# Optimization experiments

Measured on AMD Instinct MI355X. Metric: run time of the kernel, lower is better.

## Reference

```python
import jax, jax.numpy as jnp
import numpy as np

B, T, W_DIM = 32, 2048, 1024
G, D = 16, 64          # num_groups, input_dim (w = G*D)
MOM = 0.9
TH = 0.5
EPS = 1e-8
TOP_K = 2


def setup_inputs() -> dict:
    key = jax.random.key(0)
    k = jax.random.split(key, 4)
    x = jax.random.normal(k[0], (B, T, W_DIM), dtype=jnp.float32)
    ema = jnp.zeros((W_DIM, W_DIM), dtype=jnp.float32)
    W1 = jax.random.normal(k[1], (G, 16, D), dtype=jnp.float32) * 0.05
    b1 = jnp.zeros((G, 16), dtype=jnp.float32)
    W2 = jax.random.normal(k[2], (G, 1, 16), dtype=jnp.float32) * 0.05
    b2 = jnp.zeros((G, 1), dtype=jnp.float32)
    return {"x": x, "ema": ema, "W1": W1, "b1": b1, "W2": W2, "b2": b2}


def _corr_over_T(x):
    # x: (B, T, w) -> per-batch Pearson corr over the T axis: (B, w, w)
    Tn = x.shape[1]
    c = x - x.mean(axis=1, keepdims=True)
    cov = jnp.einsum('btw,btv->bwv', c, c) / (Tn - 1)
    std = jnp.sqrt(jnp.sum(c * c, axis=1) / (Tn - 1))  # (B, w)
    return jnp.clip(cov / (std[:, :, None] * std[:, None, :] + EPS), -1.0, 1.0)


def reference(x, ema, W1, b1, W2, b2):
    # --- burst-masked EMA update (torch.no_grad) ---
    corr_batch = jax.lax.stop_gradient(_corr_over_T(x))  # (B, w, w)

    def step(e, c):
        mask = jnp.abs(c) > TH
        return jnp.where(mask, MOM * e + (1.0 - MOM) * c, e), None

    ema_new, _ = jax.lax.scan(step, ema, corr_batch)

    # --- split into groups: (B, T, G, D) ---
    Bn, Tn, w = x.shape
    groups = x.reshape(Bn, Tn, G, D)

    # --- per-group correlation score: mean |off-diagonal| of within-group corr ---
    cg = groups - groups.mean(axis=1, keepdims=True)
    cov_g = jnp.einsum('btgd,btge->bgde', cg, cg) / (Tn - 1)        # (B, G, D, D)
    std_g = jnp.sqrt(jnp.sum(cg * cg, axis=1) / (Tn - 1))           # (B, G, D)
    corr_g = jnp.clip(cov_g / (std_g[..., :, None] * std_g[..., None, :] + EPS), -1.0, 1.0)
    absc = jnp.abs(corr_g)
    offdiag = (absc.sum(axis=(-2, -1)) - jnp.einsum('bgdd->bg', absc)) / (D * D - D)
    correlations = offdiag.mean(axis=0)                              # (G,)

    # --- select the 2 least-correlated groups (these get gradients) ---
    _, sel = jax.lax.top_k(-correlations, TOP_K)
    sel_mask = jnp.zeros((G,), dtype=bool).at[sel].set(True)

    # --- per-group expert MLP: D -> 16 -> 1, batched over groups ---
    h = jax.nn.relu(jnp.einsum('btgd,ghd->btgh', groups, W1) + b1)   # (B, T, G, 16)
    o = (jnp.einsum('btgh,goh->btgo', h, W2) + b2)[..., 0]           # (B, T, G)

    # non-selected groups run under no_grad -> stop_gradient on their outputs
    out = jnp.where(sel_mask[None, None, :], o, jax.lax.stop_gradient(o))
    return out, correlations, ema_new
```

## Files before the change

kernel.cpp:

```cpp
#include <hip/hip_runtime.h>
#include <hip/hip_bf16.h>
#include <stdint.h>

#define B_   32
#define T_   2048
#define W_   1024
#define G_   16
#define D_   64
#define LIST_CAP 65536

typedef __bf16 bf16_t;
typedef __bf16 bf16x8 __attribute__((ext_vector_type(8)));
typedef float  f32x4  __attribute__((ext_vector_type(4)));

#define WS_XT      0ull
#define WS_XT_SZ   (134217728ull)
#define WS_SUM     (WS_XT + WS_XT_SZ)
#define WS_SQ      (WS_SUM + 131072ull)
#define WS_MU      (WS_SQ  + 131072ull)
#define WS_SIG     (WS_MU  + 131072ull)
#define WS_ACCUM   (WS_SIG + 131072ull)
#define WS_LISTCNT (WS_ACCUM + 256ull)
#define WS_LIST    (WS_LISTCNT + 256ull)
#define WS_MASK    (WS_LIST + 1048576ull)
#define WS_DIAG    (WS_MASK + 4194304ull)

__global__ __launch_bounds__(256) void stats_transpose(
    const float* __restrict__ x, bf16_t* __restrict__ xT,
    float* __restrict__ sumb, float* __restrict__ sqb) {
  int b = blockIdx.z, t0 = blockIdx.x * 64, w0 = blockIdx.y * 64;
  __shared__ float tile[64][65];
  __shared__ float red[2][256];
  int tid = threadIdx.x;
  int c = tid & 63, r0 = tid >> 6;
  float ps = 0.f, pq = 0.f;
  const float* xp = x + ((size_t)b * T_ + t0) * W_ + w0 + c;
#pragma unroll
  for (int r = r0; r < 64; r += 4) {
    float v = xp[(size_t)r * W_];
    ps += v; pq += v * v;
    tile[c][r] = v;
  }
  red[0][tid] = ps; red[1][tid] = pq;
  __syncthreads();
  if (tid < 64) {
    float s = red[0][tid] + red[0][tid + 64] + red[0][tid + 128] + red[0][tid + 192];
    float q = red[1][tid] + red[1][tid + 64] + red[1][tid + 128] + red[1][tid + 192];
    atomicAdd(&sumb[b * W_ + w0 + tid], s);
    atomicAdd(&sqb[b * W_ + w0 + tid], q);
  }
  int tl = tid & 63, wl0 = tid >> 6;
  bf16_t* xtp = xT + ((size_t)b * W_ + w0) * T_ + t0 + tl;
#pragma unroll
  for (int wl = wl0; wl < 64; wl += 4)
    xtp[(size_t)wl * T_] = (bf16_t)tile[wl][tl];
}

__global__ void finalize_stats(const float* __restrict__ sumb,
                               const float* __restrict__ sqb,
                               float* __restrict__ mu, float* __restrict__ sig) {
  int idx = blockIdx.x * 256 + threadIdx.x;
  float s = sumb[idx], q = sqb[idx];
  float m = s * (1.0f / 2048.0f);
  float var = (q - s * m) * (1.0f / 2047.0f);
  if (var < 0.f) var = 0.f;
  mu[idx] = m;
  sig[idx] = sqrtf(var);
}

__global__ __launch_bounds__(256) void gram_kernel(
    const bf16_t* __restrict__ xT, const float* __restrict__ mu,
    const float* __restrict__ sig, unsigned int* __restrict__ mask,
    float* __restrict__ diagv, int* __restrict__ listcnt,
    int4* __restrict__ list, float* __restrict__ accum) {
  int b = blockIdx.y;
  int r = blockIdx.x, ti = 0;
  while (r >= 8 - ti) { r -= 8 - ti; ++ti; }
  int tj = ti + r;
  int i0 = ti * 128, j0 = tj * 128;

  const bf16_t* Ag = xT + ((size_t)b * W_ + i0) * T_;
  const bf16_t* Bg = xT + ((size_t)b * W_ + j0) * T_;

  __shared__ __attribute__((aligned(16))) bf16_t As[128 * 32];
  __shared__ __attribute__((aligned(16))) bf16_t Bs[128 * 32];

  int tid = threadIdx.x;
  int lane = tid & 63, wave = tid >> 6;
  int wm = wave >> 1, wn = wave & 1;

  f32x4 zero = {0.f, 0.f, 0.f, 0.f};
  f32x4 acc[4][4];
#pragma unroll
  for (int mi = 0; mi < 4; ++mi)
#pragma unroll
    for (int nj = 0; nj < 4; ++nj) acc[mi][nj] = zero;

  int aoff = (wm * 64 + (lane & 15)) * 32 + (lane >> 4) * 8;
  int boff = (wn * 64 + (lane & 15)) * 32 + (lane >> 4) * 8;

  for (int k0 = 0; k0 < T_; k0 += 32) {
    __syncthreads();
#pragma unroll
    for (int s = 0; s < 2; ++s) {
      int chunk = s * 256 + tid;
      int row = chunk >> 2, kc = (chunk & 3) * 8;
      __builtin_amdgcn_global_load_lds(
          (const __attribute__((address_space(1))) void*)(Ag + (size_t)row * T_ + k0 + kc),
          (__attribute__((address_space(3))) void*)(As + chunk * 8), 16, 0, 0);
      __builtin_amdgcn_global_load_lds(
          (const __attribute__((address_space(1))) void*)(Bg + (size_t)row * T_ + k0 + kc),
          (__attribute__((address_space(3))) void*)(Bs + chunk * 8), 16, 0, 0);
    }
    __syncthreads();

    bf16x8 af[4], bfr[4];
#pragma unroll
    for (int mi = 0; mi < 4; ++mi) af[mi]  = *(const bf16x8*)(As + aoff + mi * 512);
#pragma unroll
    for (int nj = 0; nj < 4; ++nj) bfr[nj] = *(const bf16x8*)(Bs + boff + nj * 512);
#pragma unroll
    for (int mi = 0; mi < 4; ++mi)
#pragma unroll
      for (int nj = 0; nj < 4; ++nj)
        acc[mi][nj] = __builtin_amdgcn_mfma_f32_16x16x32_bf16(af[mi], bfr[nj], acc[mi][nj], 0, 0, 0);
  }

  const float inv = 1.0f / 2047.0f;
  const float* mub = mu + b * W_;
  const float* sgb = sig + b * W_;
  bool diagquad = (ti == tj) && (wm == wn);
  float gsum = 0.f;

#pragma unroll
  for (int nj = 0; nj < 4; ++nj) {
    int j = j0 + wn * 64 + nj * 16 + (lane & 15);
    float muj = mub[j], sgj = sgb[j];
#pragma unroll
    for (int mi = 0; mi < 4; ++mi) {
#pragma unroll
      for (int rr = 0; rr < 4; ++rr) {
        int i = i0 + wm * 64 + mi * 16 + (lane >> 4) * 4 + rr;
        float cov = (acc[mi][nj][rr] - 2048.0f * mub[i] * muj) * inv;
        float corr = cov / (sgb[i] * sgj + 1e-8f);
        corr = fminf(1.0f, fmaxf(-1.0f, corr));
        if (diagquad && (i != j)) gsum += fabsf(corr);
        if (fabsf(corr) > 0.5f) {
          atomicOr(&mask[i * W_ + j], 1u << b);
          if (i == j) {
            diagv[b * W_ + i] = corr;
          } else {
            int p = atomicAdd(listcnt, 1);
            if (p < LIST_CAP) list[p] = make_int4(b, i, j, __float_as_int(corr));
          }
          if (ti != tj) {
            atomicOr(&mask[j * W_ + i], 1u << b);
            int p = atomicAdd(listcnt, 1);
            if (p < LIST_CAP) list[p] = make_int4(b, j, i, __float_as_int(corr));
          }
        }
      }
    }
  }
  if (diagquad) {
    for (int o = 32; o > 0; o >>= 1) gsum += __shfl_down(gsum, o);
    if (lane == 0) atomicAdd(&accum[ti * 2 + wm], gsum);
  }
}

__global__ void ema_kernel(const float* __restrict__ ema,
                           const unsigned int* __restrict__ mask,
                           const float* __restrict__ diagv,
                           const int* __restrict__ listcnt,
                           const int4* __restrict__ list,
                           float* __restrict__ emaout) {
  int idx = blockIdx.x * 256 + threadIdx.x;
  int i = idx >> 10, j = idx & 1023;
  float e = ema[idx];
  unsigned int m = mask[idx];
  if (m) {
    if (i == j) {
      for (int b = 0; b < 32; ++b)
        if ((m >> b) & 1u) e = 0.9f * e + 0.1f * diagv[b * W_ + i];
    } else {
      int cnt = *listcnt; if (cnt > LIST_CAP) cnt = LIST_CAP;
      for (int b = 0; b < 32; ++b) {
        if ((m >> b) & 1u) {
          for (int k = 0; k < cnt; ++k) {
            int4 t = list[k];
            if (t.x == b && t.y == i && t.z == j) {
              e = 0.9f * e + 0.1f * __int_as_float(t.w);
              break;
            }
          }
        }
      }
    }
  }
  emaout[idx] = e;
}

__global__ void corr_finalize(const float* __restrict__ accum, float* __restrict__ outc) {
  int g = threadIdx.x;
  if (g < 16) outc[g] = accum[g] * (1.0f / (32.0f * 4032.0f));
}

__global__ __launch_bounds__(256) void mlp_kernel(
    const float* __restrict__ x, const float* __restrict__ W1,
    const float* __restrict__ b1, const float* __restrict__ W2,
    const float* __restrict__ b2, float* __restrict__ out) {
  int b = blockIdx.y, t0 = blockIdx.x * 64, gs = blockIdx.z * 4;
  int tid = threadIdx.x;
  int gl = tid & 3, tl = tid >> 2;
  __shared__ float Wt[16 * 64 * 4];
  __shared__ float b1s[16 * 4], W2s[16 * 4], b2s[4];
  for (int l = tid; l < 4096; l += 256) {
    int g2 = l & 3, jd = l >> 2;
    Wt[l] = W1[(size_t)(gs + g2) * 1024 + jd];
  }
  if (tid < 64) {
    int g2 = tid & 3, j = tid >> 2;
    b1s[j * 4 + g2] = b1[(gs + g2) * 16 + j];
    W2s[j * 4 + g2] = W2[(gs + g2) * 16 + j];
  }
  if (tid < 4) b2s[tid] = b2[gs + tid];
  __syncthreads();

  int g = gs + gl, t = t0 + tl;
  const float4* xp = (const float4*)(x + ((size_t)b * T_ + t) * W_ + g * D_);
  float h[16];
#pragma unroll
  for (int j = 0; j < 16; ++j) h[j] = b1s[j * 4 + gl];
#pragma unroll
  for (int d4 = 0; d4 < 16; ++d4) {
    float4 xv = xp[d4];
#pragma unroll
    for (int j = 0; j < 16; ++j) {
      const float* wp = &Wt[(j * 64 + d4 * 4) * 4 + gl];
      h[j] += xv.x * wp[0] + xv.y * wp[4] + xv.z * wp[8] + xv.w * wp[12];
    }
  }
  float o = b2s[gl];
#pragma unroll
  for (int j = 0; j < 16; ++j) o += fmaxf(h[j], 0.f) * W2s[j * 4 + gl];
  out[((size_t)b * T_ + t) * 16 + g] = o;
}

extern "C" void kernel_launch(void* const* d_in, const int* in_sizes, int n_in,
                              void* d_out, int out_size, void* d_ws, size_t ws_size,
                              hipStream_t stream) {
  const float* x   = (const float*)d_in[0];
  const float* ema = (const float*)d_in[1];
  const float* W1  = (const float*)d_in[2];
  const float* b1  = (const float*)d_in[3];
  const float* W2  = (const float*)d_in[4];
  const float* b2  = (const float*)d_in[5];

  float* out    = (float*)d_out;
  float* outc   = out + 1048576;
  float* outema = outc + 16;

  char* ws = (char*)d_ws;
  bf16_t* xT        = (bf16_t*)(ws + WS_XT);
  float* sumb       = (float*)(ws + WS_SUM);
  float* sqb        = (float*)(ws + WS_SQ);
  float* mub        = (float*)(ws + WS_MU);
  float* sigb       = (float*)(ws + WS_SIG);
  float* accum      = (float*)(ws + WS_ACCUM);
  int*   listcnt    = (int*)(ws + WS_LISTCNT);
  int4*  list       = (int4*)(ws + WS_LIST);
  unsigned int* msk = (unsigned int*)(ws + WS_MASK);
  float* diagv      = (float*)(ws + WS_DIAG);

  hipMemsetAsync(ws + WS_SUM, 0, 262144, stream);
  hipMemsetAsync(ws + WS_ACCUM, 0, 512, stream);
  hipMemsetAsync(ws + WS_MASK, 0, 4194304, stream);

  stats_transpose<<<dim3(32, 16, 32), 256, 0, stream>>>(x, xT, sumb, sqb);
  finalize_stats<<<128, 256, 0, stream>>>(sumb, sqb, mub, sigb);
  gram_kernel<<<dim3(36, 32), 256, 0, stream>>>(xT, mub, sigb, msk, diagv, listcnt, list, accum);
  ema_kernel<<<4096, 256, 0, stream>>>(ema, msk, diagv, listcnt, list, outema);
  corr_finalize<<<1, 16, 0, stream>>>(accum, outc);
  mlp_kernel<<<dim3(32, 32, 4), 256, 0, stream>>>(x, W1, b1, W2, b2, out);
}
```

Measured before the change: 762.2 us.

## Vectorize transpose stores, double gram K-tile with XOR-swizzled LDS, XCD-aware block mapping

The stats/transpose kernel now reads x with float4 loads and writes the bf16 transpose as 16-byte vectors instead of scalar stores. The gram kernel's K tile doubles from 32 to 64, halving the number of barrier-separated iterations, and uses an XOR swizzle on LDS slots to avoid bank conflicts on fragment reads. Blocks are remapped onto a 1D grid so that each XCD handles whole batches, aiming to improve L2 reuse of each batch's xT rows. LDS use per block doubles, which may reduce occupancy.

```diff
diff --git a/kernel.cpp b/kernel.cpp
--- a/kernel.cpp
+++ b/kernel.cpp
@@ -8,6 +8,7 @@
 #define G_   16
 #define D_   64
 #define LIST_CAP 65536
+#define BK   64
 
 typedef __bf16 bf16_t;
 typedef __bf16 bf16x8 __attribute__((ext_vector_type(8)));
@@ -30,30 +31,44 @@
     float* __restrict__ sumb, float* __restrict__ sqb) {
   int b = blockIdx.z, t0 = blockIdx.x * 64, w0 = blockIdx.y * 64;
   __shared__ float tile[64][65];
-  __shared__ float red[2][256];
+  __shared__ float rs[64][17], rq[64][17];
   int tid = threadIdx.x;
-  int c = tid & 63, r0 = tid >> 6;
-  float ps = 0.f, pq = 0.f;
-  const float* xp = x + ((size_t)b * T_ + t0) * W_ + w0 + c;
-#pragma unroll
-  for (int r = r0; r < 64; r += 4) {
-    float v = xp[(size_t)r * W_];
-    ps += v; pq += v * v;
-    tile[c][r] = v;
-  }
-  red[0][tid] = ps; red[1][tid] = pq;
+  int wc = tid & 15, tr = tid >> 4;
+  float4 s4 = {0.f, 0.f, 0.f, 0.f}, q4 = {0.f, 0.f, 0.f, 0.f};
+  const float4* xp = (const float4*)(x + ((size_t)b * T_ + t0) * W_ + w0);
+#pragma unroll
+  for (int p = 0; p < 4; ++p) {
+    int t = tr + 16 * p;
+    float4 v = xp[(size_t)t * 256 + wc];
+    s4.x += v.x; s4.y += v.y; s4.z += v.z; s4.w += v.w;
+    q4.x += v.x * v.x; q4.y += v.y * v.y; q4.z += v.z * v.z; q4.w += v.w * v.w;
+    tile[4 * wc + 0][t] = v.x;
+    tile[4 * wc + 1][t] = v.y;
+    tile[4 * wc + 2][t] = v.z;
+    tile[4 * wc + 3][t] = v.w;
+  }
+  rs[4 * wc + 0][tr] = s4.x; rs[4 * wc + 1][tr] = s4.y;
+  rs[4 * wc + 2][tr] = s4.z; rs[4 * wc + 3][tr] = s4.w;
+  rq[4 * wc + 0][tr] = q4.x; rq[4 * wc + 1][tr] = q4.y;
+  rq[4 * wc + 2][tr] = q4.z; rq[4 * wc + 3][tr] = q4.w;
   __syncthreads();
   if (tid < 64) {
-    float s = red[0][tid] + red[0][tid + 64] + red[0][tid + 128] + red[0][tid + 192];
-    float q = red[1][tid] + red[1][tid + 64] + red[1][tid + 128] + red[1][tid + 192];
+    float s = 0.f, q = 0.f;
+#pragma unroll
+    for (int i = 0; i < 16; ++i) { s += rs[tid][i]; q += rq[tid][i]; }
     atomicAdd(&sumb[b * W_ + w0 + tid], s);
     atomicAdd(&sqb[b * W_ + w0 + tid], q);
   }
-  int tl = tid & 63, wl0 = tid >> 6;
-  bf16_t* xtp = xT + ((size_t)b * W_ + w0) * T_ + t0 + tl;
-#pragma unroll
-  for (int wl = wl0; wl < 64; wl += 4)
-    xtp[(size_t)wl * T_] = (bf16_t)tile[wl][tl];
+  int c = tid & 7, wv = tid >> 3;
+#pragma unroll
+  for (int p = 0; p < 2; ++p) {
+    int w = wv + 32 * p;
+    const float* src = &tile[w][c * 8];
+    bf16x8 o;
+#pragma unroll
+    for (int k = 0; k < 8; ++k) o[k] = (bf16_t)src[k];
+    *(bf16x8*)(xT + ((size_t)b * W_ + w0 + w) * T_ + t0 + c * 8) = o;
+  }
 }
 
 __global__ void finalize_stats(const float* __restrict__ sumb,
@@ -73,8 +88,13 @@
     const float* __restrict__ sig, unsigned int* __restrict__ mask,
     float* __restrict__ diagv, int* __restrict__ listcnt,
     int4* __restrict__ list, float* __restrict__ accum) {
-  int b = blockIdx.y;
-  int r = blockIdx.x, ti = 0;
+  int id = blockIdx.x;
+  int xcd = id & 7;
+  int idx = id >> 3;
+  int sub = idx / 36;
+  int rt  = idx % 36;
+  int b = sub * 8 + xcd;
+  int r = rt, ti = 0;
   while (r >= 8 - ti) { r -= 8 - ti; ++ti; }
   int tj = ti + r;
   int i0 = ti * 128, j0 = tj * 128;
@@ -82,8 +102,8 @@
   const bf16_t* Ag = xT + ((size_t)b * W_ + i0) * T_;
   const bf16_t* Bg = xT + ((size_t)b * W_ + j0) * T_;
 
-  __shared__ __attribute__((aligned(16))) bf16_t As[128 * 32];
-  __shared__ __attribute__((aligned(16))) bf16_t Bs[128 * 32];
+  __shared__ __attribute__((aligned(16))) bf16_t As[128 * BK];
+  __shared__ __attribute__((aligned(16))) bf16_t Bs[128 * BK];
 
   int tid = threadIdx.x;
   int lane = tid & 63, wave = tid >> 6;
@@ -96,34 +116,45 @@
 #pragma unroll
     for (int nj = 0; nj < 4; ++nj) acc[mi][nj] = zero;
 
-  int aoff = (wm * 64 + (lane & 15)) * 32 + (lane >> 4) * 8;
-  int boff = (wn * 64 + (lane & 15)) * 32 + (lane >> 4) * 8;
-
-  for (int k0 = 0; k0 < T_; k0 += 32) {
+  int arow = wm * 64 + (lane & 15);
+  int brow = wn * 64 + (lane & 15);
+  int q = lane >> 4;
+
+  for (int k0 = 0; k0 < T_; k0 += BK) {
     __syncthreads();
 #pragma unroll
-    for (int s = 0; s < 2; ++s) {
-      int chunk = s * 256 + tid;
-      int row = chunk >> 2, kc = (chunk & 3) * 8;
+    for (int s = 0; s < 4; ++s) {
+      int c = s * 256 + tid;
+      int row = c >> 3, slot = c & 7;
+      int gslot = slot ^ (row & 7);
       __builtin_amdgcn_global_load_lds(
-          (const __attribute__((address_space(1))) void*)(Ag + (size_t)row * T_ + k0 + kc),
-          (__attribute__((address_space(3))) void*)(As + chunk * 8), 16, 0, 0);
+          (const __attribute__((address_space(1))) void*)(Ag + (size_t)row * T_ + k0 + gslot * 8),
+          (__attribute__((address_space(3))) void*)(As + c * 8), 16, 0, 0);
       __builtin_amdgcn_global_load_lds(
-          (const __attribute__((address_space(1))) void*)(Bg + (size_t)row * T_ + k0 + kc),
-          (__attribute__((address_space(3))) void*)(Bs + chunk * 8), 16, 0, 0);
+          (const __attribute__((address_space(1))) void*)(Bg + (size_t)row * T_ + k0 + gslot * 8),
+          (__attribute__((address_space(3))) void*)(Bs + c * 8), 16, 0, 0);
     }
     __syncthreads();
 
-    bf16x8 af[4], bfr[4];
-#pragma unroll
-    for (int mi = 0; mi < 4; ++mi) af[mi]  = *(const bf16x8*)(As + aoff + mi * 512);
-#pragma unroll
-    for (int nj = 0; nj < 4; ++nj) bfr[nj] = *(const bf16x8*)(Bs + boff + nj * 512);
-#pragma unroll
-    for (int mi = 0; mi < 4; ++mi)
-#pragma unroll
-      for (int nj = 0; nj < 4; ++nj)
-        acc[mi][nj] = __builtin_amdgcn_mfma_f32_16x16x32_bf16(af[mi], bfr[nj], acc[mi][nj], 0, 0, 0);
+#pragma unroll
+    for (int s2 = 0; s2 < 2; ++s2) {
+      bf16x8 af[4], bfr[4];
+#pragma unroll
+      for (int mi = 0; mi < 4; ++mi) {
+        int row = arow + mi * 16;
+        af[mi] = *(const bf16x8*)(As + row * BK + ((s2 * 4 + q) ^ (row & 7)) * 8);
+      }
+#pragma unroll
+      for (int nj = 0; nj < 4; ++nj) {
+        int row = brow + nj * 16;
+        bfr[nj] = *(const bf16x8*)(Bs + row * BK + ((s2 * 4 + q) ^ (row & 7)) * 8);
+      }
+#pragma unroll
+      for (int mi = 0; mi < 4; ++mi)
+#pragma unroll
+        for (int nj = 0; nj < 4; ++nj)
+          acc[mi][nj] = __builtin_amdgcn_mfma_f32_16x16x32_bf16(af[mi], bfr[nj], acc[mi][nj], 0, 0, 0);
+    }
   }
 
   const float inv = 1.0f / 2047.0f;
@@ -278,7 +309,7 @@
 
   stats_transpose<<<dim3(32, 16, 32), 256, 0, stream>>>(x, xT, sumb, sqb);
   finalize_stats<<<128, 256, 0, stream>>>(sumb, sqb, mub, sigb);
-  gram_kernel<<<dim3(36, 32), 256, 0, stream>>>(xT, mub, sigb, msk, diagv, listcnt, list, accum);
+  gram_kernel<<<1152, 256, 0, stream>>>(xT, mub, sigb, msk, diagv, listcnt, list, accum);
   ema_kernel<<<4096, 256, 0, stream>>>(ema, msk, diagv, listcnt, list, outema);
   corr_finalize<<<1, 16, 0, stream>>>(accum, outc);
   mlp_kernel<<<dim3(32, 32, 4), 256, 0, stream>>>(x, W1, b1, W2, b2, out);
```

Result: faster. 728.0 us (-4.5%).
